# Kernel tuning notes

Hardware: AMD Instinct MI355X
Metric: run time of the kernel (lower is better)

The kernel has to match this reference:

```python
import jax, jax.numpy as jnp
import numpy as np

N = 100000      # nodes
E = 1_600_000   # edges
D = 64          # input_dim == hidden_dim
H = 2           # heads
C = 64          # out channels per head
ED = 16         # edge feature dim
G = 64          # graphs in batch


def setup_inputs() -> dict:
    key = jax.random.key(0)
    ks = jax.random.split(key, 12)
    s = 0.05
    return {
        "x": jax.random.normal(ks[0], (N, D), jnp.float32),
        "edge_attr": jax.random.normal(ks[1], (E, ED), jnp.float32),
        "gn_weight": jnp.ones((D,), jnp.float32),
        "gn_bias": jnp.zeros((D,), jnp.float32),
        "gn_mean_scale": jnp.ones((D,), jnp.float32),
        "W_l": jax.random.normal(ks[2], (D, H * C), jnp.float32) * s,
        "b_l": jnp.zeros((H * C,), jnp.float32),
        "W_r": jax.random.normal(ks[3], (D, H * C), jnp.float32) * s,
        "b_r": jnp.zeros((H * C,), jnp.float32),
        "W_e": jax.random.normal(ks[4], (ED, H * C), jnp.float32) * s,
        "att": jax.random.normal(ks[5], (H, C), jnp.float32) * s,
        "bias": jnp.zeros((C,), jnp.float32),
        "edge_index": jax.random.randint(ks[6], (2, E), 0, N, jnp.int32),
        "batch": jnp.sort(jax.random.randint(ks[7], (N,), 0, G, jnp.int32)),
    }


def reference(x, edge_attr, gn_weight, gn_bias, gn_mean_scale, W_l, b_l, W_r, b_r,
              W_e, att, bias, edge_index, batch):
    eps = 1e-5
    # ---- GraphNorm: per-graph mean/var with learnable mean scale ----
    cnt = jnp.maximum(jax.ops.segment_sum(jnp.ones((N,), x.dtype), batch, G), 1.0)
    mean = jax.ops.segment_sum(x, batch, G) / cnt[:, None]          # [G, D]
    xc = x - gn_mean_scale * mean[batch]                            # [N, D]
    var = jax.ops.segment_sum(xc * xc, batch, G) / cnt[:, None]     # [G, D]
    h = xc / jnp.sqrt(var + eps)[batch] * gn_weight + gn_bias
    # ---- ReLU ----
    h = jax.nn.relu(h)
    # ---- GATv2Conv (concat=False -> head mean), add_self_loops with mean-filled edge_attr ----
    xl = (h @ W_l + b_l).reshape(N, H, C)  # source transform
    xr = (h @ W_r + b_r).reshape(N, H, C)  # target transform
    src, dst = edge_index[0], edge_index[1]
    deg = jnp.maximum(jax.ops.segment_sum(jnp.ones((E,), x.dtype), dst, N), 1.0)
    loop_attr = jax.ops.segment_sum(edge_attr, dst, N) / deg[:, None]  # [N, ED]
    idx = jnp.arange(N, dtype=src.dtype)
    src_a = jnp.concatenate([src, idx])    # [E+N]
    dst_a = jnp.concatenate([dst, idx])
    ea = jnp.concatenate([edge_attr, loop_attr], axis=0)               # [E+N, ED]
    ee = (ea @ W_e).reshape(-1, H, C)
    e = xl[src_a] + xr[dst_a] + ee                                      # [E+N, H, C]
    s = jax.nn.leaky_relu(e, 0.2)
    logit = jnp.einsum('ehc,hc->eh', s, att)                            # [E+N, H]
    # segment softmax over incoming edges of each target node
    m = jax.ops.segment_max(logit, dst_a, N)                            # [N, H]
    ev = jnp.exp(logit - m[dst_a])
    denom = jax.ops.segment_sum(ev, dst_a, N)
    alpha = ev / (denom[dst_a] + 1e-16)                                 # [E+N, H]
    msg = alpha[:, :, None] * xl[src_a]                                 # [E+N, H, C]
    out = jax.ops.segment_sum(msg, dst_a, N)                            # [N, H, C]
    return out.mean(axis=1) + bias                                      # [N, C]
```

## Files before the change

kernel.cpp:

```cpp
#include <hip/hip_runtime.h>
#include <hip/hip_fp16.h>

#define NN 100000
#define NE 1600000
#define NA (NE + NN)
#define DD 64
#define HH 2
#define CC 64
#define HC 128
#define EDIM 16
#define NG 64

static const long OFF_CNT = 0;
static const long OFF_SUM = 64;
static const long OFF_VAR = OFF_SUM + 64 * 64;
static const long OFF_A   = OFF_VAR + 64 * 64;
static const long OFF_B   = OFF_A + 64 * 64;
static const long OFF_DEG = OFF_B + 64 * 64;
static const long OFF_LA  = OFF_DEG + NN;
static const long OFF_DEN = OFF_LA + (long)NN * EDIM;
static const long ZEND    = OFF_DEN + (long)NN * HH;
static const long OFF_LOG = ZEND;
static const long OFF_XL  = OFF_LOG + (long)NA * HH;
static const long OFF_XR  = OFF_XL + (long)NN * HC / 2;

__global__ void k_init(float* __restrict__ ws, float* __restrict__ out,
                       const float* __restrict__ bias) {
    long stride = (long)gridDim.x * blockDim.x;
    long i0 = (long)blockIdx.x * blockDim.x + threadIdx.x;
    for (long i = i0; i < ZEND; i += stride) ws[i] = 0.f;
    for (long i = i0; i < (long)NN * CC; i += stride) out[i] = bias[i & 63];
}

__global__ void k_gn_sum(const float* __restrict__ x, const int* __restrict__ batch,
                         float* __restrict__ sumx, float* __restrict__ cnt) {
    const int d = threadIdx.x;
    int n0 = blockIdx.x * 128;
    if (n0 >= NN) return;
    int n1 = min(n0 + 128, NN);
    int curg = batch[n0];
    float acc = 0.f, cacc = 0.f;
    for (int n = n0; n < n1; ++n) {
        int g = batch[n];
        if (g != curg) {
            atomicAdd(&sumx[curg * DD + d], acc);
            if (d == 0) atomicAdd(&cnt[curg], cacc);
            curg = g; acc = 0.f; cacc = 0.f;
        }
        acc += x[(long)n * DD + d];
        cacc += 1.f;
    }
    atomicAdd(&sumx[curg * DD + d], acc);
    if (d == 0) atomicAdd(&cnt[curg], cacc);
}

__global__ void k_gn_var(const float* __restrict__ x, const int* __restrict__ batch,
                         const float* __restrict__ sumx, const float* __restrict__ cnt,
                         const float* __restrict__ ms, float* __restrict__ varx) {
    const int d = threadIdx.x;
    int n0 = blockIdx.x * 128;
    if (n0 >= NN) return;
    int n1 = min(n0 + 128, NN);
    float msd = ms[d];
    int curg = batch[n0];
    float cg = fmaxf(cnt[curg], 1.f);
    float mu = msd * (sumx[curg * DD + d] / cg);
    float acc = 0.f;
    for (int n = n0; n < n1; ++n) {
        int g = batch[n];
        if (g != curg) {
            atomicAdd(&varx[curg * DD + d], acc);
            curg = g; acc = 0.f;
            cg = fmaxf(cnt[curg], 1.f);
            mu = msd * (sumx[curg * DD + d] / cg);
        }
        float xc = x[(long)n * DD + d] - mu;
        acc += xc * xc;
    }
    atomicAdd(&varx[curg * DD + d], acc);
}

__global__ void k_gn_ab(const float* __restrict__ sumx, const float* __restrict__ varx,
                        const float* __restrict__ cnt, const float* __restrict__ w,
                        const float* __restrict__ b, const float* __restrict__ ms,
                        float* __restrict__ A, float* __restrict__ B) {
    int i = blockIdx.x * 256 + threadIdx.x;
    if (i >= NG * DD) return;
    int g = i >> 6, d = i & 63;
    float cg = fmaxf(cnt[g], 1.f);
    float mu = ms[d] * (sumx[i] / cg);
    float a = w[d] * rsqrtf(varx[i] / cg + 1e-5f);
    A[i] = a;
    B[i] = b[d] - mu * a;
}

__global__ __launch_bounds__(128) void k_gemm(
    const float* __restrict__ x, const int* __restrict__ batch,
    const float* __restrict__ A, const float* __restrict__ B,
    const float* __restrict__ Wl, const float* __restrict__ bl,
    const float* __restrict__ Wr, const float* __restrict__ br,
    __half* __restrict__ xl, __half* __restrict__ xr) {
    __shared__ float hs[16 * 64];
    const int t = threadIdx.x;
    float wlr[64], wrr[64];
#pragma unroll
    for (int d = 0; d < 64; ++d) {
        wlr[d] = Wl[d * HC + t];
        wrr[d] = Wr[d * HC + t];
    }
    float blv = bl[t], brv = br[t];
    const long n0 = (long)blockIdx.x * 16;
    for (int e = t; e < 16 * 64; e += 128) {
        int i = e >> 6, d = e & 63;
        int g = batch[n0 + i];
        float hv = x[n0 * 64 + e] * A[g * 64 + d] + B[g * 64 + d];
        hs[e] = fmaxf(hv, 0.f);
    }
    __syncthreads();
    const float4* h4 = (const float4*)hs;
    const long co = (long)(t & 63) * 2 + (t >> 6);
    for (int i = 0; i < 16; ++i) {
        float al = blv, ar = brv;
#pragma unroll
        for (int q = 0; q < 16; ++q) {
            float4 hv = h4[i * 16 + q];
            al += hv.x * wlr[q * 4 + 0] + hv.y * wlr[q * 4 + 1] +
                  hv.z * wlr[q * 4 + 2] + hv.w * wlr[q * 4 + 3];
            ar += hv.x * wrr[q * 4 + 0] + hv.y * wrr[q * 4 + 1] +
                  hv.z * wrr[q * 4 + 2] + hv.w * wrr[q * 4 + 3];
        }
        xl[(n0 + i) * HC + co] = __float2half_rn(al);
        xr[(n0 + i) * HC + co] = __float2half_rn(ar);
    }
}

__global__ void k_loopattr(const int* __restrict__ ei, const float* __restrict__ eattr,
                           float* __restrict__ deg, float* __restrict__ la) {
    long tid = (long)blockIdx.x * 256 + threadIdx.x;
    long stride = (long)gridDim.x * 256;
    for (long i = tid; i < (long)NE * EDIM; i += stride) {
        long e = i >> 4;
        int k = (int)(i & 15);
        int d = ei[NE + e];
        atomicAdd(&la[(long)d * EDIM + k], eattr[i]);
        if (k == 0) atomicAdd(&deg[d], 1.f);
    }
}

__global__ __launch_bounds__(256) void k_logits(
    const int* __restrict__ ei, const float* __restrict__ eattr,
    const float* __restrict__ We, const float* __restrict__ att,
    const float* __restrict__ deg, const float* __restrict__ la,
    const __half2* __restrict__ xl2, const __half2* __restrict__ xr2,
    float2* __restrict__ logit) {
    __shared__ float we_s[EDIM * HC];
    for (int i = threadIdx.x; i < EDIM * HC; i += 256) we_s[i] = We[i];
    __syncthreads();
    const int lane = threadIdx.x & 63;
    const int wid = threadIdx.x >> 6;
    const float a0 = att[lane], a1 = att[64 + lane];
    long w = (long)blockIdx.x * 4 + wid;
    long nw = (long)gridDim.x * 4;
    const long NP = NA / 2;
    for (long p = w; p < NP; p += nw) {
        const long e0 = 2 * p, e1 = 2 * p + 1;
        int s0, d0, s1, d1;
        float ea0, ea1;
        if (e0 < NE) {
            s0 = ei[e0]; d0 = ei[NE + e0];
            s1 = ei[e1]; d1 = ei[NE + e1];
            ea0 = eattr[e0 * EDIM + (lane & 15)];
            ea1 = eattr[e1 * EDIM + (lane & 15)];
        } else {
            int n0 = (int)(e0 - NE), n1 = (int)(e1 - NE);
            s0 = d0 = n0; s1 = d1 = n1;
            ea0 = la[(long)n0 * EDIM + (lane & 15)] / fmaxf(deg[n0], 1.f);
            ea1 = la[(long)n1 * EDIM + (lane & 15)] / fmaxf(deg[n1], 1.f);
        }
        float2 xl0 = __half22float2(xl2[(long)s0 * 64 + lane]);
        float2 xr0 = __half22float2(xr2[(long)d0 * 64 + lane]);
        float2 xl1 = __half22float2(xl2[(long)s1 * 64 + lane]);
        float2 xr1 = __half22float2(xr2[(long)d1 * 64 + lane]);
        float ee00 = 0.f, ee01 = 0.f, ee10 = 0.f, ee11 = 0.f;
#pragma unroll
        for (int k = 0; k < 16; ++k) {
            float ak0 = __shfl(ea0, k);
            float ak1 = __shfl(ea1, k);
            float w0 = we_s[k * HC + lane];
            float w1 = we_s[k * HC + 64 + lane];
            ee00 += ak0 * w0; ee01 += ak0 * w1;
            ee10 += ak1 * w0; ee11 += ak1 * w1;
        }
        float v00 = xl0.x + xr0.x + ee00;
        float v01 = xl0.y + xr0.y + ee01;
        float v10 = xl1.x + xr1.x + ee10;
        float v11 = xl1.y + xr1.y + ee11;
        v00 = v00 > 0.f ? v00 : 0.2f * v00;
        v01 = v01 > 0.f ? v01 : 0.2f * v01;
        v10 = v10 > 0.f ? v10 : 0.2f * v10;
        v11 = v11 > 0.f ? v11 : 0.2f * v11;
        float p00 = v00 * a0, p01 = v01 * a1;
        float p10 = v10 * a0, p11 = v11 * a1;
#pragma unroll
        for (int off = 32; off > 0; off >>= 1) {
            p00 += __shfl_xor(p00, off);
            p01 += __shfl_xor(p01, off);
            p10 += __shfl_xor(p10, off);
            p11 += __shfl_xor(p11, off);
        }
        if (lane == 0) logit[e0] = make_float2(p00, p01);
        if (lane == 1) logit[e1] = make_float2(p10, p11);
    }
}

__global__ void k_denom(const int* __restrict__ ei, float2* __restrict__ logit,
                        float* __restrict__ denom) {
    long i0 = (long)blockIdx.x * 256 + threadIdx.x;
    long stride = (long)gridDim.x * 256;
    for (long e = i0; e < NA; e += stride) {
        int d2 = (e < NE) ? ei[NE + e] : (int)(e - NE);
        float2 lv = logit[e];
        float ev0 = __expf(lv.x);
        float ev1 = __expf(lv.y);
        logit[e] = make_float2(ev0, ev1);
        atomicAdd(&denom[d2 * 2 + 0], ev0);
        atomicAdd(&denom[d2 * 2 + 1], ev1);
    }
}

__global__ __launch_bounds__(256) void k_scatter(
    const int* __restrict__ ei, const float2* __restrict__ ev,
    const float2* __restrict__ denom, const __half2* __restrict__ xl2,
    float* __restrict__ out) {
    const int lane = threadIdx.x & 63;
    const int wid = threadIdx.x >> 6;
    long w = (long)blockIdx.x * 4 + wid;
    long nw = (long)gridDim.x * 4;
    const long NP = NA / 2;
    for (long p = w; p < NP; p += nw) {
        const long e0 = 2 * p, e1 = 2 * p + 1;
        int s0, d0, s1, d1;
        if (e0 < NE) {
            s0 = ei[e0]; d0 = ei[NE + e0];
            s1 = ei[e1]; d1 = ei[NE + e1];
        } else {
            s0 = d0 = (int)(e0 - NE);
            s1 = d1 = (int)(e1 - NE);
        }
        float2 ev0 = ev[e0], ev1 = ev[e1];
        float2 dn0 = denom[d0], dn1 = denom[d1];
        float2 x0 = __half22float2(xl2[(long)s0 * 64 + lane]);
        float2 x1 = __half22float2(xl2[(long)s1 * 64 + lane]);
        float al00 = ev0.x / (dn0.x + 1e-16f);
        float al01 = ev0.y / (dn0.y + 1e-16f);
        float al10 = ev1.x / (dn1.x + 1e-16f);
        float al11 = ev1.y / (dn1.y + 1e-16f);
        atomicAdd(&out[(long)d0 * CC + lane], 0.5f * (al00 * x0.x + al01 * x0.y));
        atomicAdd(&out[(long)d1 * CC + lane], 0.5f * (al10 * x1.x + al11 * x1.y));
    }
}

extern "C" void kernel_launch(void* const* d_in, const int* in_sizes, int n_in,
                              void* d_out, int out_size, void* d_ws, size_t ws_size,
                              hipStream_t stream) {
    const float* x    = (const float*)d_in[0];
    const float* eatt = (const float*)d_in[1];
    const float* gw   = (const float*)d_in[2];
    const float* gb   = (const float*)d_in[3];
    const float* gms  = (const float*)d_in[4];
    const float* Wl   = (const float*)d_in[5];
    const float* bl   = (const float*)d_in[6];
    const float* Wr   = (const float*)d_in[7];
    const float* br   = (const float*)d_in[8];
    const float* We   = (const float*)d_in[9];
    const float* att  = (const float*)d_in[10];
    const float* bias = (const float*)d_in[11];
    const int*   ei   = (const int*)d_in[12];
    const int*   batch= (const int*)d_in[13];
    float* out = (float*)d_out;
    float* ws = (float*)d_ws;

    float* cnt  = ws + OFF_CNT;
    float* sumx = ws + OFF_SUM;
    float* varx = ws + OFF_VAR;
    float* A    = ws + OFF_A;
    float* B    = ws + OFF_B;
    float* deg  = ws + OFF_DEG;
    float* la   = ws + OFF_LA;
    float* den  = ws + OFF_DEN;
    float* logit= ws + OFF_LOG;
    __half* xl  = (__half*)(ws + OFF_XL);
    __half* xr  = (__half*)(ws + OFF_XR);

    hipLaunchKernelGGL(k_init, dim3(2048), dim3(256), 0, stream, ws, out, bias);
    hipLaunchKernelGGL(k_gn_sum, dim3((NN + 127) / 128), dim3(64), 0, stream,
                       x, batch, sumx, cnt);
    hipLaunchKernelGGL(k_gn_var, dim3((NN + 127) / 128), dim3(64), 0, stream,
                       x, batch, sumx, cnt, gms, varx);
    hipLaunchKernelGGL(k_gn_ab, dim3(16), dim3(256), 0, stream,
                       sumx, varx, cnt, gw, gb, gms, A, B);
    hipLaunchKernelGGL(k_gemm, dim3(NN / 16), dim3(128), 0, stream,
                       x, batch, A, B, Wl, bl, Wr, br, xl, xr);
    hipLaunchKernelGGL(k_loopattr, dim3(4096), dim3(256), 0, stream, ei, eatt, deg, la);
    hipLaunchKernelGGL(k_logits, dim3(4096), dim3(256), 0, stream,
                       ei, eatt, We, att, deg, la,
                       (const __half2*)xl, (const __half2*)xr, (float2*)logit);
    hipLaunchKernelGGL(k_denom, dim3(4096), dim3(256), 0, stream,
                       ei, (float2*)logit, den);
    hipLaunchKernelGGL(k_scatter, dim3(4096), dim3(256), 0, stream,
                       ei, (const float2*)logit, (const float2*)den,
                       (const __half2*)xl, out);
}
```

Before: 1.602 ms.

## Fuse GraphNorm variance into one pass and exp/denominator into logits kernel

Replaces the two-pass GraphNorm mean/variance with a single pass that accumulates sum and sum of squares, then derives the variance algebraically in k_gn_ab. The exp and per-destination denominator atomics move into the logits kernel, which removes the separate k_denom pass that re-read and re-wrote the logit buffer. Grid sizes are also raised and GraphNorm blocks shrink to 16 nodes for more parallelism. The sum-of-squares variance is less numerically stable, and the exp is still taken without subtracting the segment max, as in the code before.

```diff
diff --git a/kernel.cpp b/kernel.cpp
--- a/kernel.cpp
+++ b/kernel.cpp
@@ -13,8 +13,8 @@
 
 static const long OFF_CNT = 0;
 static const long OFF_SUM = 64;
-static const long OFF_VAR = OFF_SUM + 64 * 64;
-static const long OFF_A   = OFF_VAR + 64 * 64;
+static const long OFF_SUM2= OFF_SUM + 64 * 64;
+static const long OFF_A   = OFF_SUM2 + 64 * 64;
 static const long OFF_B   = OFF_A + 64 * 64;
 static const long OFF_DEG = OFF_B + 64 * 64;
 static const long OFF_LA  = OFF_DEG + NN;
@@ -33,54 +33,31 @@
 }
 
 __global__ void k_gn_sum(const float* __restrict__ x, const int* __restrict__ batch,
-                         float* __restrict__ sumx, float* __restrict__ cnt) {
+                         float* __restrict__ sumx, float* __restrict__ sum2,
+                         float* __restrict__ cnt) {
     const int d = threadIdx.x;
-    int n0 = blockIdx.x * 128;
+    int n0 = blockIdx.x * 16;
     if (n0 >= NN) return;
-    int n1 = min(n0 + 128, NN);
+    int n1 = min(n0 + 16, NN);
     int curg = batch[n0];
-    float acc = 0.f, cacc = 0.f;
+    float a1 = 0.f, a2 = 0.f, ca = 0.f;
     for (int n = n0; n < n1; ++n) {
         int g = batch[n];
         if (g != curg) {
-            atomicAdd(&sumx[curg * DD + d], acc);
-            if (d == 0) atomicAdd(&cnt[curg], cacc);
-            curg = g; acc = 0.f; cacc = 0.f;
-        }
-        acc += x[(long)n * DD + d];
-        cacc += 1.f;
-    }
-    atomicAdd(&sumx[curg * DD + d], acc);
-    if (d == 0) atomicAdd(&cnt[curg], cacc);
-}
-
-__global__ void k_gn_var(const float* __restrict__ x, const int* __restrict__ batch,
-                         const float* __restrict__ sumx, const float* __restrict__ cnt,
-                         const float* __restrict__ ms, float* __restrict__ varx) {
-    const int d = threadIdx.x;
-    int n0 = blockIdx.x * 128;
-    if (n0 >= NN) return;
-    int n1 = min(n0 + 128, NN);
-    float msd = ms[d];
-    int curg = batch[n0];
-    float cg = fmaxf(cnt[curg], 1.f);
-    float mu = msd * (sumx[curg * DD + d] / cg);
-    float acc = 0.f;
-    for (int n = n0; n < n1; ++n) {
-        int g = batch[n];
-        if (g != curg) {
-            atomicAdd(&varx[curg * DD + d], acc);
-            curg = g; acc = 0.f;
-            cg = fmaxf(cnt[curg], 1.f);
-            mu = msd * (sumx[curg * DD + d] / cg);
-        }
-        float xc = x[(long)n * DD + d] - mu;
-        acc += xc * xc;
-    }
-    atomicAdd(&varx[curg * DD + d], acc);
-}
-
-__global__ void k_gn_ab(const float* __restrict__ sumx, const float* __restrict__ varx,
+            atomicAdd(&sumx[curg * DD + d], a1);
+            atomicAdd(&sum2[curg * DD + d], a2);
+            if (d == 0) atomicAdd(&cnt[curg], ca);
+            curg = g; a1 = 0.f; a2 = 0.f; ca = 0.f;
+        }
+        float v = x[(long)n * DD + d];
+        a1 += v; a2 += v * v; ca += 1.f;
+    }
+    atomicAdd(&sumx[curg * DD + d], a1);
+    atomicAdd(&sum2[curg * DD + d], a2);
+    if (d == 0) atomicAdd(&cnt[curg], ca);
+}
+
+__global__ void k_gn_ab(const float* __restrict__ sumx, const float* __restrict__ sum2,
                         const float* __restrict__ cnt, const float* __restrict__ w,
                         const float* __restrict__ b, const float* __restrict__ ms,
                         float* __restrict__ A, float* __restrict__ B) {
@@ -88,10 +65,12 @@
     if (i >= NG * DD) return;
     int g = i >> 6, d = i & 63;
     float cg = fmaxf(cnt[g], 1.f);
-    float mu = ms[d] * (sumx[i] / cg);
-    float a = w[d] * rsqrtf(varx[i] / cg + 1e-5f);
+    float mean = sumx[i] / cg;
+    float msm = ms[d] * mean;
+    float var = fmaxf(sum2[i] / cg - 2.f * msm * mean + msm * msm, 0.f);
+    float a = w[d] * rsqrtf(var + 1e-5f);
     A[i] = a;
-    B[i] = b[d] - mu * a;
+    B[i] = b[d] - msm * a;
 }
 
 __global__ __launch_bounds__(128) void k_gemm(
@@ -152,7 +131,7 @@
     const float* __restrict__ We, const float* __restrict__ att,
     const float* __restrict__ deg, const float* __restrict__ la,
     const __half2* __restrict__ xl2, const __half2* __restrict__ xr2,
-    float2* __restrict__ logit) {
+    float2* __restrict__ evout, float* __restrict__ denom) {
     __shared__ float we_s[EDIM * HC];
     for (int i = threadIdx.x; i < EDIM * HC; i += 256) we_s[i] = We[i];
     __syncthreads();
@@ -208,23 +187,18 @@
             p10 += __shfl_xor(p10, off);
             p11 += __shfl_xor(p11, off);
         }
-        if (lane == 0) logit[e0] = make_float2(p00, p01);
-        if (lane == 1) logit[e1] = make_float2(p10, p11);
-    }
-}
-
-__global__ void k_denom(const int* __restrict__ ei, float2* __restrict__ logit,
-                        float* __restrict__ denom) {
-    long i0 = (long)blockIdx.x * 256 + threadIdx.x;
-    long stride = (long)gridDim.x * 256;
-    for (long e = i0; e < NA; e += stride) {
-        int d2 = (e < NE) ? ei[NE + e] : (int)(e - NE);
-        float2 lv = logit[e];
-        float ev0 = __expf(lv.x);
-        float ev1 = __expf(lv.y);
-        logit[e] = make_float2(ev0, ev1);
-        atomicAdd(&denom[d2 * 2 + 0], ev0);
-        atomicAdd(&denom[d2 * 2 + 1], ev1);
+        if (lane == 0) {
+            float ev0 = __expf(p00), ev1 = __expf(p01);
+            evout[e0] = make_float2(ev0, ev1);
+            atomicAdd(&denom[d0 * 2 + 0], ev0);
+            atomicAdd(&denom[d0 * 2 + 1], ev1);
+        }
+        if (lane == 1) {
+            float ev0 = __expf(p10), ev1 = __expf(p11);
+            evout[e1] = make_float2(ev0, ev1);
+            atomicAdd(&denom[d1 * 2 + 0], ev0);
+            atomicAdd(&denom[d1 * 2 + 1], ev1);
+        }
     }
 }
 
@@ -282,32 +256,28 @@
 
     float* cnt  = ws + OFF_CNT;
     float* sumx = ws + OFF_SUM;
-    float* varx = ws + OFF_VAR;
+    float* sum2 = ws + OFF_SUM2;
     float* A    = ws + OFF_A;
     float* B    = ws + OFF_B;
     float* deg  = ws + OFF_DEG;
     float* la   = ws + OFF_LA;
     float* den  = ws + OFF_DEN;
-    float* logit= ws + OFF_LOG;
+    float* evb  = ws + OFF_LOG;
     __half* xl  = (__half*)(ws + OFF_XL);
     __half* xr  = (__half*)(ws + OFF_XR);
 
-    hipLaunchKernelGGL(k_init, dim3(2048), dim3(256), 0, stream, ws, out, bias);
-    hipLaunchKernelGGL(k_gn_sum, dim3((NN + 127) / 128), dim3(64), 0, stream,
-                       x, batch, sumx, cnt);
-    hipLaunchKernelGGL(k_gn_var, dim3((NN + 127) / 128), dim3(64), 0, stream,
-                       x, batch, sumx, cnt, gms, varx);
+    hipLaunchKernelGGL(k_init, dim3(4096), dim3(256), 0, stream, ws, out, bias);
+    hipLaunchKernelGGL(k_gn_sum, dim3((NN + 15) / 16), dim3(64), 0, stream,
+                       x, batch, sumx, sum2, cnt);
     hipLaunchKernelGGL(k_gn_ab, dim3(16), dim3(256), 0, stream,
-                       sumx, varx, cnt, gw, gb, gms, A, B);
+                       sumx, sum2, cnt, gw, gb, gms, A, B);
     hipLaunchKernelGGL(k_gemm, dim3(NN / 16), dim3(128), 0, stream,
                        x, batch, A, B, Wl, bl, Wr, br, xl, xr);
-    hipLaunchKernelGGL(k_loopattr, dim3(4096), dim3(256), 0, stream, ei, eatt, deg, la);
-    hipLaunchKernelGGL(k_logits, dim3(4096), dim3(256), 0, stream,
+    hipLaunchKernelGGL(k_loopattr, dim3(8192), dim3(256), 0, stream, ei, eatt, deg, la);
+    hipLaunchKernelGGL(k_logits, dim3(8192), dim3(256), 0, stream,
                        ei, eatt, We, att, deg, la,
-                       (const __half2*)xl, (const __half2*)xr, (float2*)logit);
-    hipLaunchKernelGGL(k_denom, dim3(4096), dim3(256), 0, stream,
-                       ei, (float2*)logit, den);
-    hipLaunchKernelGGL(k_scatter, dim3(4096), dim3(256), 0, stream,
-                       ei, (const float2*)logit, (const float2*)den,
+                       (const __half2*)xl, (const __half2*)xr, (float2*)evb, den);
+    hipLaunchKernelGGL(k_scatter, dim3(8192), dim3(256), 0, stream,
+                       ei, (const float2*)evb, (const float2*)den,
                        (const __half2*)xl, out);
 }
```

Result: faster. 1.406 ms (-12.3%).
